# Kernel tuning notes

Measured on AMD Instinct MI355X. Metric: run time of the kernel, lower is better.

## Reference

```python
import jax, jax.numpy as jnp
import numpy as np
import math

D = 1024      # input/embed dim
H = 16        # heads
HD = D // H   # head dim
FF = 4096     # feedforward dim
B, S = 2, 2048
LN_EPS = 1e-5
NEG = -9e15


def setup_inputs() -> dict:
    key = jax.random.key(0)
    ks = jax.random.split(key, 16)
    inp = {
        "x": jax.random.normal(ks[0], (B, S, D), jnp.float32),
        "mask": jax.random.randint(ks[1], (1, 1, S, S), 0, 2, jnp.int32),
        "pos_bias": jax.random.normal(ks[2], (1, H, S, S), jnp.float32),
        "sinusoidal_pos": jax.random.normal(ks[3], (1, 1, S, HD), jnp.float32),
        # params (xavier-ish scale)
        "Wqkv": jax.random.normal(ks[4], (D, 3 * D), jnp.float32) * math.sqrt(2.0 / (D + 3 * D)),
        "bqkv": jnp.zeros((3 * D,), jnp.float32),
        "Wo": jax.random.normal(ks[5], (D, D), jnp.float32) * math.sqrt(1.0 / D),
        "bo": jnp.zeros((D,), jnp.float32),
        "W1": jax.random.normal(ks[6], (D, FF), jnp.float32) * math.sqrt(2.0 / (D + FF)),
        "b1": jnp.zeros((FF,), jnp.float32),
        "W2": jax.random.normal(ks[7], (FF, D), jnp.float32) * math.sqrt(2.0 / (D + FF)),
        "b2": jnp.zeros((D,), jnp.float32),
        "g1": jnp.ones((D,), jnp.float32),
        "be1": jnp.zeros((D,), jnp.float32),
        "g2": jnp.ones((D,), jnp.float32),
        "be2": jnp.zeros((D,), jnp.float32),
    }
    return inp


def _layernorm(x, g, b):
    mu = jnp.mean(x, axis=-1, keepdims=True)
    var = jnp.mean(jnp.square(x - mu), axis=-1, keepdims=True)
    return (x - mu) * jax.lax.rsqrt(var + LN_EPS) * g + b


def _rotate_half(x):
    # x: [..., HD] -> reshape [..., 2, HD//2], swap with negation, concat
    r = x.reshape(*x.shape[:-1], 2, -1)
    x1, x2 = r[..., 0, :], r[..., 1, :]
    return jnp.concatenate([-x2, x1], axis=-1)


def _rope(x, sp):
    # sp: [1,1,S,HD]; x: [B,H,S,HD]
    return x * jnp.cos(sp) + _rotate_half(x) * jnp.sin(sp)


def reference(x, mask, pos_bias, sinusoidal_pos, Wqkv, bqkv, Wo, bo,
              W1, b1, W2, b2, g1, be1, g2, be2):
    # pre-norm (note: residual uses the normalized x, matching the source)
    x = _layernorm(x, g1, be1)
    b, s, d = x.shape
    qkv = (x @ Wqkv + bqkv).reshape(b, s, H, 3 * HD).transpose(0, 2, 1, 3)
    q, k, v = jnp.split(qkv, 3, axis=-1)  # each [B,H,S,HD]
    sp = sinusoidal_pos[:, :, -s:]
    q = _rope(q, sp)
    k = _rope(k, sp)
    logits = jnp.einsum("bhqd,bhkd->bhqk", q, k)
    logits = (logits + pos_bias) / math.sqrt(HD)
    logits = jnp.where(mask == 0, NEG, logits)
    attn = jax.nn.softmax(logits, axis=-1)
    vals = jnp.einsum("bhqk,bhkd->bhqd", attn, v)
    vals = vals.transpose(0, 2, 1, 3).reshape(b, s, d)
    attn_out = vals @ Wo + bo
    x = x + attn_out
    x = _layernorm(x, g2, be2)
    h = jax.nn.gelu(x @ W1 + b1, approximate=False)  # torch GELU is exact
    x = x + (h @ W2 + b2)
    return x
```

## Files before the change

### kernel.cpp

```cpp
#include <hip/hip_runtime.h>
#include <math.h>

#define DD   1024
#define HH   16
#define HDD  64
#define FFF  4096
#define NB   2
#define NS   2048
#define NR   (NB * NS)
#define TDQ  (3 * DD)
#define NKT  (NS / 64)
#define NSP  2

typedef __attribute__((ext_vector_type(8))) _Float16 hfrag;
typedef __attribute__((ext_vector_type(4))) _Float16 h4v;
typedef __attribute__((ext_vector_type(16))) float f32x16;
typedef __attribute__((ext_vector_type(8))) unsigned short us8;
typedef __attribute__((ext_vector_type(4))) unsigned int u32x4;

__device__ __forceinline__ float4 ld4(const float* p) {
    return *reinterpret_cast<const float4*>(p);
}
__device__ __forceinline__ float gelu_f(float x) {
    return 0.5f * x * (1.0f + erff(x * 0.70710678118654752440f));
}
#define MFMA32H(a, b, c) __builtin_amdgcn_mfma_f32_32x32x16_f16((a), (b), (c), 0, 0, 0)

__global__ __launch_bounds__(256) void ln_kernel(const float* __restrict__ in,
        const float* __restrict__ gw, const float* __restrict__ bw,
        float* __restrict__ outf, _Float16* __restrict__ oh) {
    int row = blockIdx.x;
    float4 v = reinterpret_cast<const float4*>(in + (size_t)row * DD)[threadIdx.x];
    float s1 = v.x + v.y + v.z + v.w;
    float s2 = v.x * v.x + v.y * v.y + v.z * v.z + v.w * v.w;
#pragma unroll
    for (int off = 1; off < 64; off <<= 1) {
        s1 += __shfl_xor(s1, off);
        s2 += __shfl_xor(s2, off);
    }
    __shared__ float r1[4], r2[4];
    int wid = threadIdx.x >> 6;
    if ((threadIdx.x & 63) == 0) { r1[wid] = s1; r2[wid] = s2; }
    __syncthreads();
    s1 = r1[0] + r1[1] + r1[2] + r1[3];
    s2 = r2[0] + r2[1] + r2[2] + r2[3];
    float mu   = s1 * (1.0f / DD);
    float var  = s2 * (1.0f / DD) - mu * mu;
    float rstd = rsqrtf(var + 1e-5f);
    float4 g = reinterpret_cast<const float4*>(gw)[threadIdx.x];
    float4 b = reinterpret_cast<const float4*>(bw)[threadIdx.x];
    float o[4];
    o[0] = (v.x - mu) * rstd * g.x + b.x;
    o[1] = (v.y - mu) * rstd * g.y + b.y;
    o[2] = (v.z - mu) * rstd * g.z + b.z;
    o[3] = (v.w - mu) * rstd * g.w + b.w;
    float4 of; of.x = o[0]; of.y = o[1]; of.z = o[2]; of.w = o[3];
    reinterpret_cast<float4*>(outf + (size_t)row * DD)[threadIdx.x] = of;
    h4v hv;
#pragma unroll
    for (int j = 0; j < 4; ++j) hv[j] = (_Float16)o[j];
    *reinterpret_cast<h4v*>(oh + (size_t)row * DD + threadIdx.x * 4) = hv;
}

__global__ __launch_bounds__(256) void wt_convert(const float* __restrict__ W,
        _Float16* __restrict__ Th, int K, int N) {
    __shared__ float s[32][33];
    int tx = threadIdx.x & 31, ty = threadIdx.x >> 5;
    int n0 = blockIdx.x * 32, k0 = blockIdx.y * 32;
#pragma unroll
    for (int i = 0; i < 4; ++i)
        s[ty + i * 8][tx] = W[(size_t)(k0 + ty + i * 8) * N + n0 + tx];
    __syncthreads();
#pragma unroll
    for (int i = 0; i < 4; ++i) {
        int n = n0 + ty + i * 8;
        Th[(size_t)n * K + k0 + tx] = (_Float16)s[tx][ty + i * 8];
    }
}

__global__ __launch_bounds__(256) void cs_table(const float* __restrict__ sp,
        float* __restrict__ ct, float* __restrict__ st) {
    int i = blockIdx.x * 256 + threadIdx.x;
    float v = sp[i];
    ct[i] = cosf(v);
    st[i] = sinf(v);
}

__global__ __launch_bounds__(256) void mask8(const int* __restrict__ mask,
        unsigned char* __restrict__ mb) {
    int i = blockIdx.x * 256 + threadIdx.x;
    int4 v = reinterpret_cast<const int4*>(mask)[i];
    unsigned int o = (unsigned int)(v.x & 1) | ((unsigned int)(v.y & 1) << 8)
                   | ((unsigned int)(v.z & 1) << 16) | ((unsigned int)(v.w & 1) << 24);
    reinterpret_cast<unsigned int*>(mb)[i] = o;
}

__global__ __launch_bounds__(256) void rope_split(const _Float16* __restrict__ qkv,
        const float* __restrict__ ct, const float* __restrict__ st,
        _Float16* __restrict__ Qp, _Float16* __restrict__ Kp, _Float16* __restrict__ Vt) {
    __shared__ _Float16 sv[64][72];
    const int t = threadIdx.x;
    const int tile = blockIdx.x, bh = blockIdx.y;
    const int b = bh >> 4, h = bh & 15;
    const int r = t >> 2, p = t & 3;
    const int srow = tile * 64 + r;
    const _Float16* base = qkv + ((size_t)(b * NS + srow)) * TDQ + h * 192;

#pragma unroll
    for (int qk = 0; qk < 2; ++qk) {
        const _Float16* src = base + qk * 64;
        hfrag va = *reinterpret_cast<const hfrag*>(src + p * 8);
        hfrag vc = *reinterpret_cast<const hfrag*>(src + 32 + p * 8);
        hfrag o1, o2;
#pragma unroll
        for (int j = 0; j < 8; ++j) {
            int d1 = p * 8 + j, d2 = 32 + p * 8 + j;
            float a = (float)va[j], c = (float)vc[j];
            float c1 = ct[(size_t)srow * HDD + d1], s1 = st[(size_t)srow * HDD + d1];
            float c2 = ct[(size_t)srow * HDD + d2], s2 = st[(size_t)srow * HDD + d2];
            o1[j] = (_Float16)(a * c1 - c * s1);
            o2[j] = (_Float16)(c * c2 + a * s2);
        }
        _Float16* dst = qk ? Kp : Qp;
        size_t obase = ((size_t)bh * NS + srow) * HDD;
        *reinterpret_cast<hfrag*>(dst + obase + p * 8)      = o1;
        *reinterpret_cast<hfrag*>(dst + obase + 32 + p * 8) = o2;
    }
    const _Float16* vsrc = base + 128;
    hfrag v0 = *reinterpret_cast<const hfrag*>(vsrc + p * 16);
    hfrag v1 = *reinterpret_cast<const hfrag*>(vsrc + p * 16 + 8);
#pragma unroll
    for (int j = 0; j < 8; ++j) {
        sv[p * 16 + j][r]     = v0[j];
        sv[p * 16 + 8 + j][r] = v1[j];
    }
    __syncthreads();
    {
        int d = t >> 2, kb = (t & 3) * 16;
        size_t obase = ((size_t)bh * HDD + d) * NS + tile * 64 + kb;
        *reinterpret_cast<hfrag*>(Vt + obase)     = *reinterpret_cast<hfrag*>(&sv[d][kb]);
        *reinterpret_cast<hfrag*>(Vt + obase + 8) = *reinterpret_cast<hfrag*>(&sv[d][kb + 8]);
    }
}

__global__ __launch_bounds__(256) void attn_mfma(
        const _Float16* __restrict__ Qp, const _Float16* __restrict__ Kp,
        const _Float16* __restrict__ Vt,
        const float* __restrict__ pos_bias, const unsigned char* __restrict__ maskb,
        float* __restrict__ Opart, float2* __restrict__ Lpart) {
    __shared__ _Float16 kT[2][64][72];
    __shared__ _Float16 vT[2][64][72];
    __shared__ _Float16 PBs[4][32][68];
    const int t = threadIdx.x;
    const int w = t >> 6, lane = t & 63, lq = lane & 31, hi = lane >> 5;
    const int h = blockIdx.y;
    const int qt = blockIdx.x, sp = blockIdx.z;
    const int q0 = qt * 128;
    const int qg = q0 + 32 * w + lq;
    const int sw = ((lq >> 3) & 3) << 3;
    const int KT0 = sp * (NKT / NSP), KT1 = KT0 + (NKT / NSP);
    const float C1  = 0.18033688011112042f;
    const float THR = 11.5f;

    hfrag qf[2][4];
#pragma unroll
    for (int bt = 0; bt < 2; ++bt)
#pragma unroll
        for (int dk = 0; dk < 4; ++dk)
            qf[bt][dk] = *reinterpret_cast<const hfrag*>(
                Qp + ((size_t)(bt * HH + h) * NS + qg) * HDD + 16 * dk + 8 * hi);

    f32x16 o[2][2];
#pragma unroll
    for (int bt = 0; bt < 2; ++bt) { o[bt][0] = (f32x16)0.0f; o[bt][1] = (f32x16)0.0f; }
    float mrun[2] = { -INFINITY, -INFINITY }, lsum[2] = { 0.0f, 0.0f };

    const int sr0 = t >> 2, sc = t & 3;
    const int swr = ((sr0 >> 3) & 3) << 3;
    const int brow = lane >> 4;
    const int bcol = (lane & 15) * 4;
    us8 kr[2][2], vr[2][2];
    float4 pbr[8]; unsigned int pmk[8];

#define STAGE_LOAD(KT) {                                                        \
        int kv0_ = (KT) * 64;                                                   \
        _Pragma("unroll")                                                       \
        for (int bt = 0; bt < 2; ++bt) {                                        \
            size_t kb_ = ((size_t)(bt * HH + h) * NS + kv0_ + sr0) * HDD + 16 * sc; \
            size_t vb_ = ((size_t)(bt * HH + h) * HDD + sr0) * NS + kv0_ + 16 * sc; \
            kr[bt][0] = *reinterpret_cast<const us8*>(Kp + kb_);                \
            kr[bt][1] = *reinterpret_cast<const us8*>(Kp + kb_ + 8);            \
            vr[bt][0] = *reinterpret_cast<const us8*>(Vt + vb_);                \
            vr[bt][1] = *reinterpret_cast<const us8*>(Vt + vb_ + 8);            \
        }                                                                       \
        _Pragma("unroll")                                                       \
        for (int i = 0; i < 8; ++i) {                                           \
            int rg_ = q0 + 32 * w + brow + 4 * i;                               \
            pbr[i] = ld4(pos_bias + ((size_t)h * NS + rg_) * NS + kv0_ + bcol); \
            pmk[i] = *reinterpret_cast<const unsigned int*>(                    \
                         maskb + (size_t)rg_ * NS + kv0_ + bcol);               \
        }                                                                       \
    }

    STAGE_LOAD(KT0);
    for (int kt = KT0; kt < KT1; ++kt) {
        __syncthreads();
#pragma unroll
        for (int bt = 0; bt < 2; ++bt) {
            *reinterpret_cast<us8*>(&kT[bt][sr0][(16 * sc) ^ swr])     = kr[bt][0];
            *reinterpret_cast<us8*>(&kT[bt][sr0][(16 * sc + 8) ^ swr]) = kr[bt][1];
            *reinterpret_cast<us8*>(&vT[bt][sr0][(16 * sc) ^ swr])     = vr[bt][0];
            *reinterpret_cast<us8*>(&vT[bt][sr0][(16 * sc + 8) ^ swr]) = vr[bt][1];
        }
#pragma unroll
        for (int i = 0; i < 8; ++i) {
            h4v pv;
#pragma unroll
            for (int j = 0; j < 4; ++j)
                pv[j] = ((pmk[i] >> (8 * j)) & 0xffu)
                      ? (_Float16)(pbr[i][j] * C1) : (_Float16)(-60000.0f);
            *reinterpret_cast<h4v*>(&PBs[w][brow + 4 * i][bcol]) = pv;
        }
        __syncthreads();
        if (kt + 1 < KT1) STAGE_LOAD(kt + 1);

#pragma unroll
        for (int bt = 0; bt < 2; ++bt) {
            f32x16 s0 = (f32x16)0.0f, s1 = (f32x16)0.0f;
#pragma unroll
            for (int dk = 0; dk < 4; ++dk) {
                hfrag k0 = *reinterpret_cast<const hfrag*>(
                    &kT[bt][lq][(16 * dk + 8 * hi) ^ sw]);
                hfrag k1 = *reinterpret_cast<const hfrag*>(
                    &kT[bt][32 + lq][(16 * dk + 8 * hi) ^ sw]);
                s0 = MFMA32H(k0, qf[bt][dk], s0);
                s1 = MFMA32H(k1, qf[bt][dk], s1);
            }
            float sv[2][16];
#pragma unroll
            for (int m2 = 0; m2 < 2; ++m2)
#pragma unroll
                for (int g = 0; g < 4; ++g) {
                    h4v pb4 = *reinterpret_cast<const h4v*>(
                        &PBs[w][lq][32 * m2 + 8 * g + 4 * hi]);
#pragma unroll
                    for (int j = 0; j < 4; ++j) {
                        int r = 4 * g + j;
                        float sraw = (m2 == 0) ? s0[r] : s1[r];
                        sv[m2][r] = fmaf(sraw, C1, (float)pb4[j]);
                    }
                }
            float mx = sv[0][0];
#pragma unroll
            for (int m2 = 0; m2 < 2; ++m2)
#pragma unroll
                for (int r = 0; r < 16; ++r) mx = fmaxf(mx, sv[m2][r]);
            mx = fmaxf(mx, __shfl_xor(mx, 32));
            if (__any(mx > mrun[bt] + THR)) {
                float mnew = fmaxf(mrun[bt], mx);
                float corr = __builtin_amdgcn_exp2f(mrun[bt] - mnew);
                lsum[bt] *= corr;
                mrun[bt] = mnew;
#pragma unroll
                for (int r = 0; r < 16; ++r) {
                    int iq = (r & 3) + 8 * (r >> 2) + 4 * hi;
                    float cr = __shfl(corr, iq);
                    o[bt][0][r] *= cr; o[bt][1][r] *= cr;
                }
            }
            float ps = 0.0f;
            hfrag af[4];
#pragma unroll
            for (int m2 = 0; m2 < 2; ++m2)
#pragma unroll
                for (int gp = 0; gp < 2; ++gp) {
                    float p0 = __builtin_amdgcn_exp2f(sv[m2][8 * gp + 0] - mrun[bt]);
                    float p1 = __builtin_amdgcn_exp2f(sv[m2][8 * gp + 1] - mrun[bt]);
                    float p2 = __builtin_amdgcn_exp2f(sv[m2][8 * gp + 2] - mrun[bt]);
                    float p3 = __builtin_amdgcn_exp2f(sv[m2][8 * gp + 3] - mrun[bt]);
                    float p4 = __builtin_amdgcn_exp2f(sv[m2][8 * gp + 4] - mrun[bt]);
                    float p5 = __builtin_amdgcn_exp2f(sv[m2][8 * gp + 5] - mrun[bt]);
                    float p6 = __builtin_amdgcn_exp2f(sv[m2][8 * gp + 6] - mrun[bt]);
                    float p7 = __builtin_amdgcn_exp2f(sv[m2][8 * gp + 7] - mrun[bt]);
                    ps += (p0 + p1) + (p2 + p3) + (p4 + p5) + (p6 + p7);
                    unsigned int XA = __builtin_bit_cast(unsigned int, __builtin_amdgcn_cvt_pkrtz(p0, p1));
                    unsigned int XB = __builtin_bit_cast(unsigned int, __builtin_amdgcn_cvt_pkrtz(p2, p3));
                    unsigned int XC = __builtin_bit_cast(unsigned int, __builtin_amdgcn_cvt_pkrtz(p4, p5));
                    unsigned int XD = __builtin_bit_cast(unsigned int, __builtin_amdgcn_cvt_pkrtz(p6, p7));
                    unsigned int YA = (unsigned int)__shfl_xor((int)XA, 32);
                    unsigned int YB = (unsigned int)__shfl_xor((int)XB, 32);
                    unsigned int YC = (unsigned int)__shfl_xor((int)XC, 32);
                    unsigned int YD = (unsigned int)__shfl_xor((int)XD, 32);
                    u32x4 aw;
                    aw[0] = hi ? YC : XA;
                    aw[1] = hi ? YD : XB;
                    aw[2] = hi ? XC : YA;
                    aw[3] = hi ? XD : YB;
                    af[m2 * 2 + gp] = __builtin_bit_cast(hfrag, aw);
                }
            ps += __shfl_xor(ps, 32);
            lsum[bt] += ps;
#pragma unroll
            for (int kp = 0; kp < 4; ++kp) {
                hfrag v0 = *reinterpret_cast<const hfrag*>(
                    &vT[bt][lq][(16 * kp + 8 * hi) ^ sw]);
                hfrag v1 = *reinterpret_cast<const hfrag*>(
                    &vT[bt][32 + lq][(16 * kp + 8 * hi) ^ sw]);
                o[bt][0] = MFMA32H(af[kp], v0, o[bt][0]);
                o[bt][1] = MFMA32H(af[kp], v1, o[bt][1]);
            }
        }
    }
#undef STAGE_LOAD
#pragma unroll
    for (int bt = 0; bt < 2; ++bt) {
        size_t obase = (((size_t)((bt * HH + h) * 16 + qt)) * NSP + sp) * (size_t)(128 * 64);
#pragma unroll
        for (int r = 0; r < 16; ++r) {
            int iq = (r & 3) + 8 * (r >> 2) + 4 * hi;
            Opart[obase + (size_t)(32 * w + iq) * 64 + lq]      = o[bt][0][r];
            Opart[obase + (size_t)(32 * w + iq) * 64 + 32 + lq] = o[bt][1][r];
        }
        if (hi == 0) {
            float2 ml; ml.x = mrun[bt]; ml.y = lsum[bt];
            Lpart[(((size_t)((bt * HH + h) * 16 + qt)) * NSP + sp) * 128 + 32 * w + lq] = ml;
        }
    }
}

__global__ __launch_bounds__(256) void attn_combine(const float* __restrict__ Opart,
        const float2* __restrict__ Lpart, _Float16* __restrict__ valf) {
    const int qt = blockIdx.x;
    const int h = blockIdx.y >> 1, b = blockIdx.y & 1;
    const int bh = b * HH + h;
    const int t = threadIdx.x;
    const int qloc = t >> 2, d0 = (t & 3) * 16;
    size_t base = ((size_t)(bh * 16 + qt)) * NSP;
#pragma unroll
    for (int half = 0; half < 2; ++half) {
        int q = qloc + 64 * half;
        float2 ml0 = Lpart[(base + 0) * 128 + q];
        float2 ml1 = Lpart[(base + 1) * 128 + q];
        float m = fmaxf(ml0.x, ml1.x);
        float a0 = __builtin_amdgcn_exp2f(ml0.x - m);
        float a1 = __builtin_amdgcn_exp2f(ml1.x - m);
        float inv = 1.0f / (ml0.y * a0 + ml1.y * a1);
        const float* O0 = Opart + (base + 0) * 8192 + (size_t)q * 64 + d0;
        const float* O1 = Opart + (base + 1) * 8192 + (size_t)q * 64 + d0;
        _Float16* dst = valf + ((size_t)(b * NS + qt * 128 + q)) * DD + h * HDD + d0;
#pragma unroll
        for (int j = 0; j < 4; ++j) {
            float4 x0 = ld4(O0 + 4 * j), x1 = ld4(O1 + 4 * j);
            h4v o;
            o[0] = (_Float16)((x0.x * a0 + x1.x * a1) * inv);
            o[1] = (_Float16)((x0.y * a0 + x1.y * a1) * inv);
            o[2] = (_Float16)((x0.z * a0 + x1.z * a1) * inv);
            o[3] = (_Float16)((x0.w * a0 + x1.w * a1) * inv);
            *reinterpret_cast<h4v*>(dst + 4 * j) = o;
        }
    }
}

template<int EPI>
__global__ __launch_bounds__(256, 2) void gemm_h(
        const _Float16* __restrict__ A, const _Float16* __restrict__ B,
        const float* __restrict__ bias, const float* __restrict__ resid,
        float* __restrict__ Cf, _Float16* __restrict__ Ch,
        int M, int N, int K) {
    __shared__ _Float16 sA[128][72];
    __shared__ _Float16 sB[128][72];
    const int t = threadIdx.x;
    const int w = t >> 6, lane = t & 63, lq = lane & 31, hi = lane >> 5;
    const int wr = w >> 1, wc = w & 1;
    const int m0 = blockIdx.y * 128, n0 = blockIdx.x * 128;
    const int sw = ((lq >> 3) & 3) << 3;

    f32x16 acc[2][2];
#pragma unroll
    for (int m = 0; m < 2; ++m)
#pragma unroll
        for (int n = 0; n < 2; ++n) acc[m][n] = (f32x16)0.0f;

    const int sr = t >> 1, skc = (t & 1) * 16;
    const int swr = ((sr >> 3) & 3) << 3;
    const _Float16* Ap = A + (size_t)(m0 + sr) * K + skc;
    const _Float16* Bp = B + (size_t)(n0 + sr) * K + skc;

    for (int k0 = 0; k0 < K; k0 += 32) {
        us8 a0 = *reinterpret_cast<const us8*>(Ap + k0);
        us8 a1 = *reinterpret_cast<const us8*>(Ap + k0 + 8);
        us8 b0 = *reinterpret_cast<const us8*>(Bp + k0);
        us8 b1 = *reinterpret_cast<const us8*>(Bp + k0 + 8);
        __syncthreads();
        *reinterpret_cast<us8*>(&sA[sr][(skc) ^ swr])     = a0;
        *reinterpret_cast<us8*>(&sA[sr][(skc + 8) ^ swr]) = a1;
        *reinterpret_cast<us8*>(&sB[sr][(skc) ^ swr])     = b0;
        *reinterpret_cast<us8*>(&sB[sr][(skc + 8) ^ swr]) = b1;
        __syncthreads();
        hfrag fa[2][2], fb[2][2];
#pragma unroll
        for (int mb = 0; mb < 2; ++mb)
#pragma unroll
            for (int kc = 0; kc < 2; ++kc)
                fa[mb][kc] = *reinterpret_cast<const hfrag*>(
                    &sA[wr * 64 + mb * 32 + lq][(kc * 16 + 8 * hi) ^ sw]);
#pragma unroll
        for (int nb = 0; nb < 2; ++nb)
#pragma unroll
            for (int kc = 0; kc < 2; ++kc)
                fb[nb][kc] = *reinterpret_cast<const hfrag*>(
                    &sB[wc * 64 + nb * 32 + lq][(kc * 16 + 8 * hi) ^ sw]);
#pragma unroll
        for (int kc = 0; kc < 2; ++kc)
#pragma unroll
            for (int mb = 0; mb < 2; ++mb)
#pragma unroll
                for (int nb = 0; nb < 2; ++nb)
                    acc[mb][nb] = MFMA32H(fa[mb][kc], fb[nb][kc], acc[mb][nb]);
    }
#pragma unroll
    for (int mb = 0; mb < 2; ++mb)
#pragma unroll
        for (int nb = 0; nb < 2; ++nb) {
            int colg = n0 + wc * 64 + nb * 32 + lq;
            float bv = bias[colg];
#pragma unroll
            for (int r = 0; r < 16; ++r) {
                int rowg = m0 + wr * 64 + mb * 32 + (r & 3) + 8 * (r >> 2) + 4 * hi;
                float v = acc[mb][nb][r] + bv;
                if (EPI == 1) v += resid[(size_t)rowg * N + colg];
                if (EPI == 2) {
                    Ch[(size_t)rowg * N + colg] = (_Float16)gelu_f(v);
                } else if (EPI == 3) {
                    Ch[(size_t)rowg * N + colg] = (_Float16)v;
                } else {
                    Cf[(size_t)rowg * N + colg] = v;
                }
            }
        }
}

__global__ __launch_bounds__(256, 2) void gemm_h2(
        const _Float16* __restrict__ A, const _Float16* __restrict__ B,
        const float* __restrict__ bias, const float* __restrict__ resid,
        float* __restrict__ Cf, int M, int N, int K) {
    __shared__ _Float16 sA[64][72];
    __shared__ _Float16 sB[128][72];
    const int t = threadIdx.x;
    const int w = t >> 6, lane = t & 63, lq = lane & 31, hi = lane >> 5;
    const int m0 = blockIdx.y * 64, n0 = blockIdx.x * 128;
    const int sw = ((lq >> 3) & 3) << 3;

    f32x16 acc[2];
    acc[0] = (f32x16)0.0f; acc[1] = (f32x16)0.0f;

    const int ar = t >> 2, akc = (t & 3) * 8;
    const int aswr = ((ar >> 3) & 3) << 3;
    const int br = t >> 1, bkc = (t & 1) * 16;
    const int bswr = ((br >> 3) & 3) << 3;
    const _Float16* Ap = A + (size_t)(m0 + ar) * K + akc;
    const _Float16* Bp = B + (size_t)(n0 + br) * K + bkc;

    for (int k0 = 0; k0 < K; k0 += 32) {
        us8 a0 = *reinterpret_cast<const us8*>(Ap + k0);
        us8 b0 = *reinterpret_cast<const us8*>(Bp + k0);
        us8 b1 = *reinterpret_cast<const us8*>(Bp + k0 + 8);
        __syncthreads();
        *reinterpret_cast<us8*>(&sA[ar][(akc) ^ aswr])     = a0;
        *reinterpret_cast<us8*>(&sB[br][(bkc) ^ bswr])     = b0;
        *reinterpret_cast<us8*>(&sB[br][(bkc + 8) ^ bswr]) = b1;
        __syncthreads();
        hfrag fa[2][2], fb[2];
#pragma unroll
        for (int mb = 0; mb < 2; ++mb)
#pragma unroll
            for (int kc = 0; kc < 2; ++kc)
                fa[mb][kc] = *reinterpret_cast<const hfrag*>(
                    &sA[mb * 32 + lq][(kc * 16 + 8 * hi) ^ sw]);
#pragma unroll
        for (int kc = 0; kc < 2; ++kc)
            fb[kc] = *reinterpret_cast<const hfrag*>(
                &sB[32 * w + lq][(kc * 16 + 8 * hi) ^ sw]);
#pragma unroll
        for (int kc = 0; kc < 2; ++kc)
#pragma unroll
            for (int mb = 0; mb < 2; ++mb)
                acc[mb] = MFMA32H(fa[mb][kc], fb[kc], acc[mb]);
    }
    int colg = n0 + 32 * w + lq;
    float bv = bias[colg];
#pragma unroll
    for (int mb = 0; mb < 2; ++mb)
#pragma unroll
        for (int r = 0; r < 16; ++r) {
            int rowg = m0 + mb * 32 + (r & 3) + 8 * (r >> 2) + 4 * hi;
            float v = acc[mb][r] + bv + resid[(size_t)rowg * N + colg];
            Cf[(size_t)rowg * N + colg] = v;
        }
}

extern "C" void kernel_launch(void* const* d_in, const int* in_sizes, int n_in,
                              void* d_out, int out_size, void* d_ws, size_t ws_size,
                              hipStream_t stream) {
    const float* x        = (const float*)d_in[0];
    const int*   mask     = (const int*)d_in[1];
    const float* pos_bias = (const float*)d_in[2];
    const float* sp       = (const float*)d_in[3];
    const float* Wqkv     = (const float*)d_in[4];
    const float* bqkv     = (const float*)d_in[5];
    const float* Wo       = (const float*)d_in[6];
    const float* bo       = (const float*)d_in[7];
    const float* W1       = (const float*)d_in[8];
    const float* b1       = (const float*)d_in[9];
    const float* W2       = (const float*)d_in[10];
    const float* b2       = (const float*)d_in[11];
    const float* g1       = (const float*)d_in[12];
    const float* be1      = (const float*)d_in[13];
    const float* g2       = (const float*)d_in[14];
    const float* be2      = (const float*)d_in[15];
    float* out = (float*)d_out;
    char* wsb = (char*)d_ws;

    float*          xbuf  = (float*)(wsb);
    _Float16*       actF  = (_Float16*)(wsb + ((size_t)16 << 20));
    _Float16*       wT    = (_Float16*)(wsb + ((size_t)24 << 20));
    float*          ct    = (float*)(wsb + ((size_t)32 << 20));
    float*          stb   = (float*)(wsb + ((size_t)33 << 20));
    unsigned char*  mkb   = (unsigned char*)(wsb + ((size_t)34 << 20));
    _Float16*       qkvh  = (_Float16*)(wsb + ((size_t)48 << 20));
    _Float16*       Qp    = (_Float16*)(wsb + ((size_t)72 << 20));
    _Float16*       Kp    = (_Float16*)(wsb + ((size_t)80 << 20));
    _Float16*       Vt    = (_Float16*)(wsb + ((size_t)88 << 20));
    _Float16*       hF    = (_Float16*)(wsb + ((size_t)48 << 20));
    float*          Opart = (float*)(wsb + ((size_t)96 << 20));
    float2*         Lpart = (float2*)(wsb + ((size_t)130 << 20));

    ln_kernel<<<NR, 256, 0, stream>>>(x, g1, be1, xbuf, actF);
    wt_convert<<<dim3(TDQ / 32, DD / 32), 256, 0, stream>>>(Wqkv, wT, DD, TDQ);
    gemm_h<3><<<dim3(TDQ / 128, NR / 128), 256, 0, stream>>>(
        actF, wT, bqkv, nullptr, nullptr, qkvh, NR, TDQ, DD);
    cs_table<<<(NS * HDD) / 256, 256, 0, stream>>>(sp, ct, stb);
    mask8<<<(NS * NS / 4) / 256, 256, 0, stream>>>(mask, mkb);
    rope_split<<<dim3(NS / 64, NB * HH), 256, 0, stream>>>(qkvh, ct, stb, Qp, Kp, Vt);
    attn_mfma<<<dim3(NS / 128, HH, NSP), 256, 0, stream>>>(
        Qp, Kp, Vt, pos_bias, mkb, Opart, Lpart);
    attn_combine<<<dim3(NS / 128, NB * HH), 256, 0, stream>>>(Opart, Lpart, actF);
    wt_convert<<<dim3(DD / 32, DD / 32), 256, 0, stream>>>(Wo, wT, DD, DD);
    gemm_h2<<<dim3(DD / 128, NR / 64), 256, 0, stream>>>(
        actF, wT, bo, xbuf, xbuf, NR, DD, DD);
    ln_kernel<<<NR, 256, 0, stream>>>(xbuf, g2, be2, xbuf, actF);
    wt_convert<<<dim3(FFF / 32, DD / 32), 256, 0, stream>>>(W1, wT, DD, FFF);
    gemm_h<2><<<dim3(FFF / 128, NR / 128), 256, 0, stream>>>(
        actF, wT, b1, nullptr, nullptr, hF, NR, FFF, DD);
    wt_convert<<<dim3(DD / 32, FFF / 32), 256, 0, stream>>>(W2, wT, FFF, DD);
    gemm_h2<<<dim3(DD / 128, NR / 64), 256, 0, stream>>>(
        hF, wT, b2, xbuf, out, NR, DD, FFF);
}
```

Before: 406.2 us.

## Fuse RoPE and head split into QKV GEMM epilogue with fp16 cos/sin table

The QKV GEMM epilogue now applies RoPE and writes Q, K and raw V straight into per-head layouts, so the fp16 qkv intermediate and the separate rope_split pass go away. A small vtrans kernel still transposes V. The cos/sin table is packed as fp16 quads, which halves its size but rounds the rotation coefficients to fp16. Epilogue stores are scattered 2-byte writes, which may coalesce less well than the old row stores.

```diff
diff --git a/kernel.cpp b/kernel.cpp
--- a/kernel.cpp
+++ b/kernel.cpp
@@ -78,12 +78,15 @@
     }
 }
 
-__global__ __launch_bounds__(256) void cs_table(const float* __restrict__ sp,
-        float* __restrict__ ct, float* __restrict__ st) {
+__global__ __launch_bounds__(256) void cs4_table(const float* __restrict__ sp,
+        h4v* __restrict__ cs4) {
     int i = blockIdx.x * 256 + threadIdx.x;
-    float v = sp[i];
-    ct[i] = cosf(v);
-    st[i] = sinf(v);
+    int s = i >> 5, d = i & 31;
+    float a = sp[s * 64 + d], b = sp[s * 64 + d + 32];
+    h4v v;
+    v[0] = (_Float16)cosf(a); v[1] = (_Float16)sinf(a);
+    v[2] = (_Float16)cosf(b); v[3] = (_Float16)sinf(b);
+    cs4[i] = v;
 }
 
 __global__ __launch_bounds__(256) void mask8(const int* __restrict__ mask,
@@ -95,40 +98,15 @@
     reinterpret_cast<unsigned int*>(mb)[i] = o;
 }
 
-__global__ __launch_bounds__(256) void rope_split(const _Float16* __restrict__ qkv,
-        const float* __restrict__ ct, const float* __restrict__ st,
-        _Float16* __restrict__ Qp, _Float16* __restrict__ Kp, _Float16* __restrict__ Vt) {
+__global__ __launch_bounds__(256) void vtrans(const _Float16* __restrict__ Vr,
+        _Float16* __restrict__ Vt) {
     __shared__ _Float16 sv[64][72];
     const int t = threadIdx.x;
     const int tile = blockIdx.x, bh = blockIdx.y;
-    const int b = bh >> 4, h = bh & 15;
     const int r = t >> 2, p = t & 3;
-    const int srow = tile * 64 + r;
-    const _Float16* base = qkv + ((size_t)(b * NS + srow)) * TDQ + h * 192;
-
-#pragma unroll
-    for (int qk = 0; qk < 2; ++qk) {
-        const _Float16* src = base + qk * 64;
-        hfrag va = *reinterpret_cast<const hfrag*>(src + p * 8);
-        hfrag vc = *reinterpret_cast<const hfrag*>(src + 32 + p * 8);
-        hfrag o1, o2;
-#pragma unroll
-        for (int j = 0; j < 8; ++j) {
-            int d1 = p * 8 + j, d2 = 32 + p * 8 + j;
-            float a = (float)va[j], c = (float)vc[j];
-            float c1 = ct[(size_t)srow * HDD + d1], s1 = st[(size_t)srow * HDD + d1];
-            float c2 = ct[(size_t)srow * HDD + d2], s2 = st[(size_t)srow * HDD + d2];
-            o1[j] = (_Float16)(a * c1 - c * s1);
-            o2[j] = (_Float16)(c * c2 + a * s2);
-        }
-        _Float16* dst = qk ? Kp : Qp;
-        size_t obase = ((size_t)bh * NS + srow) * HDD;
-        *reinterpret_cast<hfrag*>(dst + obase + p * 8)      = o1;
-        *reinterpret_cast<hfrag*>(dst + obase + 32 + p * 8) = o2;
-    }
-    const _Float16* vsrc = base + 128;
-    hfrag v0 = *reinterpret_cast<const hfrag*>(vsrc + p * 16);
-    hfrag v1 = *reinterpret_cast<const hfrag*>(vsrc + p * 16 + 8);
+    const _Float16* src = Vr + ((size_t)bh * NS + tile * 64 + r) * HDD;
+    hfrag v0 = *reinterpret_cast<const hfrag*>(src + p * 16);
+    hfrag v1 = *reinterpret_cast<const hfrag*>(src + p * 16 + 8);
 #pragma unroll
     for (int j = 0; j < 8; ++j) {
         sv[p * 16 + j][r]     = v0[j];
@@ -366,6 +344,8 @@
         const _Float16* __restrict__ A, const _Float16* __restrict__ B,
         const float* __restrict__ bias, const float* __restrict__ resid,
         float* __restrict__ Cf, _Float16* __restrict__ Ch,
+        _Float16* __restrict__ Qp, _Float16* __restrict__ Kp,
+        _Float16* __restrict__ Vr, const h4v* __restrict__ cs4,
         int M, int N, int K) {
     __shared__ _Float16 sA[128][72];
     __shared__ _Float16 sB[128][72];
@@ -418,6 +398,37 @@
                 for (int nb = 0; nb < 2; ++nb)
                     acc[mb][nb] = MFMA32H(fa[mb][kc], fb[nb][kc], acc[mb][nb]);
     }
+    if (EPI == 4) {
+        const int b64 = blockIdx.x * 2 + wc;
+        const int qk = b64 % 3, hh = b64 / 3;
+        const float bv0 = bias[n0 + wc * 64 + lq];
+        const float bv1 = bias[n0 + wc * 64 + 32 + lq];
+#pragma unroll
+        for (int mb = 0; mb < 2; ++mb)
+#pragma unroll
+            for (int g = 0; g < 4; ++g)
+#pragma unroll
+                for (int rr = 0; rr < 4; ++rr) {
+                    int r = 4 * g + rr;
+                    int rowg = m0 + wr * 64 + mb * 32 + rr + 8 * g + 4 * hi;
+                    int s = rowg & (NS - 1), bb = rowg >> 11;
+                    float v0 = acc[mb][0][r] + bv0;
+                    float v1 = acc[mb][1][r] + bv1;
+                    _Float16* dstb = (qk == 0 ? Qp : (qk == 1 ? Kp : Vr))
+                        + ((size_t)(bb * HH + hh) * NS + s) * HDD;
+                    if (qk < 2) {
+                        h4v cs = cs4[(size_t)s * 32 + lq];
+                        float c1 = (float)cs[0], s1 = (float)cs[1];
+                        float c2 = (float)cs[2], s2 = (float)cs[3];
+                        dstb[lq]      = (_Float16)(v0 * c1 - v1 * s1);
+                        dstb[32 + lq] = (_Float16)(v1 * c2 + v0 * s2);
+                    } else {
+                        dstb[lq]      = (_Float16)v0;
+                        dstb[32 + lq] = (_Float16)v1;
+                    }
+                }
+        return;
+    }
 #pragma unroll
     for (int mb = 0; mb < 2; ++mb)
 #pragma unroll
@@ -431,8 +442,6 @@
                 if (EPI == 1) v += resid[(size_t)rowg * N + colg];
                 if (EPI == 2) {
                     Ch[(size_t)rowg * N + colg] = (_Float16)gelu_f(v);
-                } else if (EPI == 3) {
-                    Ch[(size_t)rowg * N + colg] = (_Float16)v;
                 } else {
                     Cf[(size_t)rowg * N + colg] = v;
                 }
@@ -524,10 +533,9 @@
     float*          xbuf  = (float*)(wsb);
     _Float16*       actF  = (_Float16*)(wsb + ((size_t)16 << 20));
     _Float16*       wT    = (_Float16*)(wsb + ((size_t)24 << 20));
-    float*          ct    = (float*)(wsb + ((size_t)32 << 20));
-    float*          stb   = (float*)(wsb + ((size_t)33 << 20));
+    h4v*            cs4   = (h4v*)(wsb + ((size_t)32 << 20));
     unsigned char*  mkb   = (unsigned char*)(wsb + ((size_t)34 << 20));
-    _Float16*       qkvh  = (_Float16*)(wsb + ((size_t)48 << 20));
+    _Float16*       Vr    = (_Float16*)(wsb + ((size_t)48 << 20));
     _Float16*       Qp    = (_Float16*)(wsb + ((size_t)72 << 20));
     _Float16*       Kp    = (_Float16*)(wsb + ((size_t)80 << 20));
     _Float16*       Vt    = (_Float16*)(wsb + ((size_t)88 << 20));
@@ -536,12 +544,12 @@
     float2*         Lpart = (float2*)(wsb + ((size_t)130 << 20));
 
     ln_kernel<<<NR, 256, 0, stream>>>(x, g1, be1, xbuf, actF);
+    cs4_table<<<(NS * 32) / 256, 256, 0, stream>>>(sp, cs4);
+    mask8<<<(NS * NS / 4) / 256, 256, 0, stream>>>(mask, mkb);
     wt_convert<<<dim3(TDQ / 32, DD / 32), 256, 0, stream>>>(Wqkv, wT, DD, TDQ);
-    gemm_h<3><<<dim3(TDQ / 128, NR / 128), 256, 0, stream>>>(
-        actF, wT, bqkv, nullptr, nullptr, qkvh, NR, TDQ, DD);
-    cs_table<<<(NS * HDD) / 256, 256, 0, stream>>>(sp, ct, stb);
-    mask8<<<(NS * NS / 4) / 256, 256, 0, stream>>>(mask, mkb);
-    rope_split<<<dim3(NS / 64, NB * HH), 256, 0, stream>>>(qkvh, ct, stb, Qp, Kp, Vt);
+    gemm_h<4><<<dim3(TDQ / 128, NR / 128), 256, 0, stream>>>(
+        actF, wT, bqkv, nullptr, nullptr, nullptr, Qp, Kp, Vr, cs4, NR, TDQ, DD);
+    vtrans<<<dim3(NS / 64, NB * HH), 256, 0, stream>>>(Vr, Vt);
     attn_mfma<<<dim3(NS / 128, HH, NSP), 256, 0, stream>>>(
         Qp, Kp, Vt, pos_bias, mkb, Opart, Lpart);
     attn_combine<<<dim3(NS / 128, NB * HH), 256, 0, stream>>>(Opart, Lpart, actF);
@@ -551,7 +559,8 @@
     ln_kernel<<<NR, 256, 0, stream>>>(xbuf, g2, be2, xbuf, actF);
     wt_convert<<<dim3(FFF / 32, DD / 32), 256, 0, stream>>>(W1, wT, DD, FFF);
     gemm_h<2><<<dim3(FFF / 128, NR / 128), 256, 0, stream>>>(
-        actF, wT, b1, nullptr, nullptr, hF, NR, FFF, DD);
+        actF, wT, b1, nullptr, nullptr, hF, nullptr, nullptr, nullptr, nullptr,
+        NR, FFF, DD);
     wt_convert<<<dim3(DD / 32, FFF / 32), 256, 0, stream>>>(W2, wT, FFF, DD);
     gemm_h2<<<dim3(DD / 128, NR / 64), 256, 0, stream>>>(
         hF, wT, b2, xbuf, out, NR, DD, FFF);
```

New measurement: 407.9 us. No clear change (+0.4%).
